# Performance work log

Hardware: AMD Instinct MI355X
Metric: run time of the kernel (lower is better)

## Reference

```python
import jax, jax.numpy as jnp
import numpy as np

B, S, D, H = 4, 2048, 1024, 16
DK = D // H


def setup_inputs() -> dict:
    key = jax.random.key(0)
    ks = jax.random.split(key, 16)
    s = 0.02
    inp = {
        "Q": jax.random.normal(ks[0], (B, S, D), jnp.float32),
        "K": jax.random.normal(ks[1], (B, S, D), jnp.float32),
        "V": jax.random.normal(ks[2], (B, S, D), jnp.float32),
        "mask": jax.random.randint(ks[3], (B, 1, S, S), 0, 2, jnp.int32),
        "wq": jax.random.normal(ks[4], (D, D), jnp.float32) * s,
        "bq": jnp.zeros((D,), jnp.float32),
        "wk": jax.random.normal(ks[5], (D, D), jnp.float32) * s,
        "bk": jnp.zeros((D,), jnp.float32),
        "wv": jax.random.normal(ks[6], (D, D), jnp.float32) * s,
        "bv": jnp.zeros((D,), jnp.float32),
        "wo": jax.random.normal(ks[7], (D, D), jnp.float32) * s,
        "bo": jnp.zeros((D,), jnp.float32),
        "na_q_w": jax.random.normal(ks[8], (DK, DK), jnp.float32) * 0.1,
        "na_q_b": jnp.zeros((DK,), jnp.float32),
        "na_k_w": jax.random.normal(ks[9], (DK, DK), jnp.float32) * 0.1,
        "na_k_b": jnp.zeros((DK,), jnp.float32),
        "temperature": jnp.ones((H, 1, 1), jnp.float32),
        "rms_w": jnp.ones((D,), jnp.float32),
    }
    return inp


def _split_heads(x):
    # [B,S,D] -> [B,H,S,DK]
    return x.reshape(B, S, H, DK).transpose(0, 2, 1, 3)


def reference(Q, K, V, mask, wq, bq, wk, bk, wv, bv, wo, bo,
              na_q_w, na_q_b, na_k_w, na_k_b, temperature, rms_w):
    q = _split_heads(Q @ wq.T + bq)
    k = _split_heads(K @ wk.T + bk)
    v = _split_heads(V @ wv.T + bv)
    # NeuralAttention: tanh-transformed Q,K then scaled dot product
    qn = jnp.tanh(q @ na_q_w.T + na_q_b)
    kn = jnp.tanh(k @ na_k_w.T + na_k_b)
    scores = jnp.einsum("bhqd,bhkd->bhqk", qn, kn) / (DK ** 0.5)
    scores = scores / temperature  # [H,1,1] broadcasts over [B,H,S,S]
    scores = jnp.where(mask == 0, jnp.float32(-1e9), scores)
    attn = jax.nn.softmax(scores, axis=-1)
    ctx = jnp.einsum("bhqk,bhkd->bhqd", attn, v)
    out = ctx.transpose(0, 2, 1, 3).reshape(B, S, D) @ wo.T + bo
    # RMSNorm
    out = out * jax.lax.rsqrt(jnp.mean(out * out, axis=-1, keepdims=True) + 1e-8) * rms_w
    return out
```

## Files before the change

kernel.cpp:

```cpp
#include <hip/hip_runtime.h>
#include <hip/hip_bf16.h>

constexpr int Bc  = 4;
constexpr int Sc  = 2048;
constexpr int Dc  = 1024;
constexpr int Hc  = 16;
constexpr int DKc = 64;
constexpr int Mc  = Bc * Sc;

typedef __bf16 bf16x8 __attribute__((ext_vector_type(8)));
typedef float  f32x4  __attribute__((ext_vector_type(4)));
typedef unsigned short ushort_t;

#define DEV __device__ __forceinline__

DEV unsigned short f2bf(float f) {
    unsigned u = __builtin_bit_cast(unsigned, f);
    u += 0x7FFFu + ((u >> 16) & 1u);
    return (unsigned short)(u >> 16);
}
DEV unsigned pack2(float a, float b) {
    return (unsigned)f2bf(a) | ((unsigned)f2bf(b) << 16);
}
DEV void gl16(const void* g, void* l) {
    __builtin_amdgcn_global_load_lds((const __attribute__((address_space(1))) unsigned int*)g,
                                     (__attribute__((address_space(3))) unsigned int*)l, 16, 0, 0);
}
DEV f32x4 mfma16(bf16x8 a, bf16x8 b, f32x4 c) {
    return __builtin_amdgcn_mfma_f32_16x16x32_bf16(a, b, c, 0, 0, 0);
}
DEV unsigned spread4(unsigned x) {
    x = (x | (x << 12)) & 0x000F000Fu;
    x = (x | (x << 6))  & 0x03030303u;
    x = (x | (x << 3))  & 0x11111111u;
    return x;
}


__global__ __launch_bounds__(256) void fold_w2(const float* __restrict__ naqw,
                                               const float* __restrict__ wq,
                                               unsigned short* __restrict__ wqf,
                                               const float* __restrict__ nakw,
                                               const float* __restrict__ wk,
                                               unsigned short* __restrict__ wkf,
                                               const float* __restrict__ bq,
                                               const float* __restrict__ naqb,
                                               float* __restrict__ bqf,
                                               const float* __restrict__ bk,
                                               const float* __restrict__ nakb,
                                               float* __restrict__ bkf) {
    const int colg = blockIdx.x, h = blockIdx.y, z = blockIdx.z;
    if (z == 2) {
        if (h >= 2) return;
        const float* na = h ? nakw : naqw;
        const float* b  = h ? bk : bq;
        const float* nb = h ? nakb : naqb;
        float* out      = h ? bkf : bqf;
        int idx = colg * 256 + threadIdx.x;
        if (idx >= Dc) return;
        int hh = idx >> 6, i = idx & 63;
        float acc = nb[i];
        for (int t = 0; t < DKc; ++t) acc += na[i * DKc + t] * b[hh * DKc + t];
        out[idx] = acc;
        return;
    }
    const float* na = z ? nakw : naqw;
    const float* w  = z ? wk : wq;
    unsigned short* out = z ? wkf : wqf;
    const int col = colg * 256 + threadIdx.x;

    __shared__ float nal[64 * 64];
    for (int i = threadIdx.x; i < 4096; i += 256) nal[i] = na[i];

    float wr[64];
#pragma unroll
    for (int t = 0; t < 64; ++t) wr[t] = w[(h * 64 + t) * Dc + col];
    __syncthreads();

    for (int i = 0; i < 64; ++i) {
        float acc = 0.f;
#pragma unroll
        for (int t = 0; t < 64; ++t) acc += nal[i * 64 + t] * wr[t];
        out[(h * 64 + i) * Dc + col] = f2bf(acc);
    }
}

constexpr int CONVB = (3 * Mc * Dc + 2 * Dc * Dc) / 8 / 256;
constexpr int MASKB = Bc * Sc * Sc / 1024;
__global__ __launch_bounds__(256) void conv_mask(const float* __restrict__ Q,
                                                 const float* __restrict__ K,
                                                 const float* __restrict__ V,
                                                 const float* __restrict__ wv,
                                                 const float* __restrict__ wo,
                                                 ushort_t* __restrict__ qb,
                                                 ushort_t* __restrict__ kb,
                                                 ushort_t* __restrict__ vb,
                                                 ushort_t* __restrict__ wvf,
                                                 ushort_t* __restrict__ wof,
                                                 const int* __restrict__ m,
                                                 unsigned* __restrict__ mbits) {
    const int bid = blockIdx.x;
    const int tid = threadIdx.x;
    if (bid < CONVB) {
        size_t i = ((size_t)bid * 256 + tid) * 8;
        constexpr size_t N = (size_t)Mc * Dc;
        constexpr size_t W = (size_t)Dc * Dc;
        const float* src; ushort_t* dst; size_t off;
        if      (i < N)         { src = Q;  dst = qb;  off = i; }
        else if (i < 2 * N)     { src = K;  dst = kb;  off = i - N; }
        else if (i < 3 * N)     { src = V;  dst = vb;  off = i - 2 * N; }
        else if (i < 3 * N + W) { src = wv; dst = wvf; off = i - 3 * N; }
        else                    { src = wo; dst = wof; off = i - 3 * N - W; }
        float4 a = *(const float4*)(src + off), b = *(const float4*)(src + off + 4);
        uint4 o;
        o.x = pack2(a.x, a.y); o.y = pack2(a.z, a.w);
        o.z = pack2(b.x, b.y); o.w = pack2(b.z, b.w);
        *(uint4*)(dst + off) = o;
    } else {
        const int mb = bid - CONVB;
        const size_t p0 = ((size_t)mb * 256 + tid) * 4;
        const int ing = (int)(p0 & 63);
        const int nat = (((ing >> 4) & 1) << 5) | (((ing >> 2) & 3) << 3)
                      | (((ing >> 5) & 1) << 2);
        const int4 mv = *(const int4*)(m + ((p0 & ~(size_t)63) | (size_t)nat));
        unsigned nib = (unsigned)(mv.x != 0) | ((unsigned)(mv.y != 0) << 1)
                     | ((unsigned)(mv.z != 0) << 2) | ((unsigned)(mv.w != 0) << 3);
        unsigned long long bal0 = __ballot((nib & 1u) != 0);
        unsigned long long bal1 = __ballot((nib & 2u) != 0);
        unsigned long long bal2 = __ballot((nib & 4u) != 0);
        unsigned long long bal3 = __ballot((nib & 8u) != 0);
        const int lane = tid & 63, s = tid >> 6;
        const int sh8 = (lane & 7) * 8;
        unsigned bb0 = (unsigned)(bal0 >> sh8) & 0xFFu;
        unsigned bb1 = (unsigned)(bal1 >> sh8) & 0xFFu;
        unsigned bb2 = (unsigned)(bal2 >> sh8) & 0xFFu;
        unsigned bb3 = (unsigned)(bal3 >> sh8) & 0xFFu;
        unsigned word = spread4(bb0) | (spread4(bb1) << 1)
                      | (spread4(bb2) << 2) | (spread4(bb3) << 3);
        if (lane < 8) mbits[(size_t)mb * 32 + s * 8 + lane] = word;
    }
}

template <int EPI, int SWZ>
__global__ __launch_bounds__(256) void gemm_bt(const ushort_t* __restrict__ A,
                                               const ushort_t* __restrict__ B,
                                               const float* __restrict__ bias,
                                               void* __restrict__ outp,
                                               int Mdim, int Ndim, int Kdim,
                                               const float* __restrict__ temp,
                                               const ushort_t* __restrict__ A2,
                                               const ushort_t* __restrict__ B2,
                                               const float* __restrict__ bias2,
                                               void* __restrict__ outp2) {
    __shared__ __align__(16) unsigned char As[2][16384];
    __shared__ __align__(16) unsigned char Bs[2][16384];

    int zz = 0;
    if constexpr (EPI == 4) {
        zz = blockIdx.z;
        if (zz) { A = A2; B = B2; bias = bias2; outp = outp2; }
    }

    int bx = blockIdx.x, by = blockIdx.y;
    if constexpr (SWZ != 0) {
        int nwg = gridDim.x * gridDim.y;
        int L = by * gridDim.x + bx;
        int cpx = nwg >> 3;
        int orig = (L & 7) * cpx + (L >> 3);
        if constexpr (SWZ == 1) { bx = orig % gridDim.x; by = orig / gridDim.x; }
        else                    { by = orig % gridDim.y; bx = orig / gridDim.y; }
    }

    const int tid = threadIdx.x, lane = tid & 63, wave = tid >> 6;
    const int wr = wave >> 1, wc = wave & 1;
    const int q = lane & 15, g = lane >> 4;
    const int m0 = by * 128, n0 = bx * 128;

    const int strow = lane >> 3, stcol = (lane & 7) * 8;
    const ushort_t* Ab = A + (size_t)(m0 + strow) * Kdim + stcol;
    const ushort_t* Bb = B + (size_t)(n0 + strow) * Kdim + stcol;

    f32x4 acc[4][4] = {};
    const int nK = Kdim >> 6;

#pragma unroll
    for (int i = 0; i < 4; ++i) {
        const int ro = (wave * 4 + i) * 8;
        gl16(Ab + (size_t)ro * Kdim, As[0] + (wave * 4 + i) * 1024);
        gl16(Bb + (size_t)ro * Kdim, Bs[0] + (wave * 4 + i) * 1024);
    }
    __syncthreads();

    for (int kt = 0; kt < nK; ++kt) {
        const int cur = kt & 1;
        if (kt + 1 < nK) {
            const int k1 = (kt + 1) << 6;
#pragma unroll
            for (int i = 0; i < 4; ++i) {
                const int ro = (wave * 4 + i) * 8;
                gl16(Ab + (size_t)ro * Kdim + k1, As[cur ^ 1] + (wave * 4 + i) * 1024);
                gl16(Bb + (size_t)ro * Kdim + k1, Bs[cur ^ 1] + (wave * 4 + i) * 1024);
            }
        }
#pragma unroll
        for (int s = 0; s < 2; ++s) {
            const int cb = s * 64 + g * 16;
            bf16x8 a[4], b[4];
#pragma unroll
            for (int m = 0; m < 4; ++m)
                a[m] = *(const bf16x8*)(As[cur] + (wr * 64 + m * 16 + q) * 128 + cb);
#pragma unroll
            for (int n = 0; n < 4; ++n)
                b[n] = *(const bf16x8*)(Bs[cur] + (wc * 64 + n * 16 + q) * 128 + cb);
#pragma unroll
            for (int m = 0; m < 4; ++m)
#pragma unroll
                for (int n = 0; n < 4; ++n)
                    acc[m][n] = mfma16(a[m], b[n], acc[m][n]);
        }
        __syncthreads();
    }

#pragma unroll
    for (int m = 0; m < 4; ++m)
#pragma unroll
        for (int n = 0; n < 4; ++n) {
            int gn = n0 + wc * 64 + n * 16 + q;
            float sc_h = 1.f;
            if constexpr (EPI == 0 || EPI == 4) {
                if (EPI == 0 || zz == 0)
                    sc_h = 0.18033688011112042f * __builtin_amdgcn_rcpf(temp[gn >> 6]);
            }
#pragma unroll
            for (int r = 0; r < 4; ++r) {
                int gm = m0 + wr * 64 + m * 16 + (g << 2) + r;
                float v = acc[m][n][r];
                if constexpr (EPI == 0 || EPI == 3 || EPI == 4) {
                    v = tanhf(v + bias[gn]);
                    int b = gm >> 11, s = gm & 2047, hh = gn >> 6, dk = gn & 63;
                    bool qmode = (EPI == 0) || (EPI == 4 && zz == 0);
                    if (qmode) {
                        ((unsigned short*)outp)[(((size_t)(b * Hc + hh)) * Sc + s) * DKc + dk] = f2bf(v * sc_h);
                    } else {
                        int kt2 = s >> 7, nr = s & 127;
                        int prow = (nr & 64) | (((nr >> 5) & 1) << 4) | (((nr >> 3) & 3) << 2)
                                 | (((nr >> 2) & 1) << 5) | (nr & 3);
                        int eofs = ((dk * 2) ^ ((prow & 7) << 4)) >> 1;
                        size_t idx = ((size_t)(b * Hc + hh)) * Sc * DKc + (size_t)kt2 * 8192 + prow * 64 + eofs;
                        ((unsigned short*)outp)[idx] = f2bf(v);
                    }
                } else if constexpr (EPI == 1) {
                    v += bias[gm];
                    int hh = gm >> 6, dk = gm & 63, b = gn >> 11, s = gn & 2047;
                    int kt2 = s >> 7, kloc = s & 127;
                    int eofs = ((kloc * 2) ^ ((dk & 7) << 4)) >> 1;
                    size_t idx = ((size_t)(b * Hc + hh)) * Sc * DKc + (size_t)kt2 * 8192 + dk * 128 + eofs;
                    ((unsigned short*)outp)[idx] = f2bf(v);
                } else {
                    v += bias[gn];
                    ((float*)outp)[(size_t)gm * Ndim + gn] = v;
                }
            }
        }
}

__global__ __launch_bounds__(512, 2) void attn_k(const ushort_t* __restrict__ qn,
                                                 const ushort_t* __restrict__ kn,
                                                 const ushort_t* __restrict__ vtp,
                                                 const unsigned* __restrict__ mbits,
                                                 ushort_t* __restrict__ ctxb) {
    __shared__ __align__(16) unsigned char Kl[2][16384];
    __shared__ __align__(16) unsigned char Vl[2][16384];

    const int tid = threadIdx.x, lane = tid & 63, wave = tid >> 6;
    const int q = lane & 15, g = lane >> 4;

    const int wg = blockIdx.x;
    const int orig = (wg & 7) * 64 + (wg >> 3);
    const int qt = orig & 7, h = (orig >> 3) & 15, b = orig >> 7;
    const int q0 = qt * 256;
    const int qr0 = q0 + wave * 32 + q;
    const size_t headoff = ((size_t)(b * Hc + h)) * Sc * DKc;

    const unsigned char* Ksrc = (const unsigned char*)(kn + headoff);
    const unsigned char* Vsrc = (const unsigned char*)(vtp + headoff);
    const int so = wave * 1024 + lane * 16;
    const int ld = wave * 1024;

    bf16x8 qf[2][2];
    {
        const ushort_t* p0 = qn + headoff + (size_t)qr0 * DKc + g * 8;
        qf[0][0] = *(const bf16x8*)p0;
        qf[0][1] = *(const bf16x8*)(p0 + 32);
        qf[1][0] = *(const bf16x8*)(p0 + 16 * DKc);
        qf[1][1] = *(const bf16x8*)(p0 + 16 * DKc + 32);
    }
    const unsigned* mr0 = mbits + ((size_t)b * Sc + qr0) * (Sc / 32);
    const unsigned* mr1 = mr0 + 16 * (Sc / 32);

    bf16x8 ones;
#pragma unroll
    for (int i = 0; i < 8; ++i) ones[i] = (__bf16)1.0f;

    f32x4 ctxa[2][4] = {};
    f32x4 lacc[2] = {};
    const int swz = (q & 7) << 4;
    const int sh = g << 2;

    gl16(Ksrc + so,        &Kl[0][ld]);
    gl16(Ksrc + 8192 + so, &Kl[0][8192 + ld]);
    gl16(Vsrc + so,        &Vl[0][ld]);
    gl16(Vsrc + 8192 + so, &Vl[0][8192 + ld]);
    __syncthreads();

    for (int kt = 0; kt < Sc / 128; ++kt) {
        const int cur = kt & 1;
        if (kt < Sc / 128 - 1) {
            const unsigned char* ks = Ksrc + (kt + 1) * 16384;
            const unsigned char* vs = Vsrc + (kt + 1) * 16384;
            gl16(ks + so,        &Kl[cur ^ 1][ld]);
            gl16(ks + 8192 + so, &Kl[cur ^ 1][8192 + ld]);
            gl16(vs + so,        &Vl[cur ^ 1][ld]);
            gl16(vs + 8192 + so, &Vl[cur ^ 1][8192 + ld]);
        }
        unsigned mwq[2][4];
        {
            uint4 t0 = *(const uint4*)(mr0 + kt * 4);
            uint4 t1 = *(const uint4*)(mr1 + kt * 4);
            mwq[0][0] = t0.x >> sh; mwq[0][1] = t0.y >> sh;
            mwq[0][2] = t0.z >> sh; mwq[0][3] = t0.w >> sh;
            mwq[1][0] = t1.x >> sh; mwq[1][1] = t1.y >> sh;
            mwq[1][2] = t1.z >> sh; mwq[1][3] = t1.w >> sh;
        }
        const unsigned char* Kb = Kl[cur];
        const unsigned char* Vb = Vl[cur];

#pragma unroll
        for (int kh = 0; kh < 2; ++kh) {
            f32x4 s0[4] = {}, s1[4] = {};
            __builtin_amdgcn_s_setprio(1);
#pragma unroll
            for (int f = 0; f < 4; ++f) {
                const int ro = (kh * 64 + f * 16 + q) * 128;
                bf16x8 a0 = *(const bf16x8*)(Kb + ro + ((g * 16) ^ swz));
                bf16x8 a1 = *(const bf16x8*)(Kb + ro + ((64 + g * 16) ^ swz));
                s0[f] = mfma16(a0, qf[0][0], s0[f]);
                s0[f] = mfma16(a1, qf[0][1], s0[f]);
                s1[f] = mfma16(a0, qf[1][0], s1[f]);
                s1[f] = mfma16(a1, qf[1][1], s1[f]);
            }
            __builtin_amdgcn_s_setprio(0);

#pragma unroll
            for (int f = 0; f < 4; ++f) {
                unsigned w0 = mwq[0][kh * 2 + (f >> 1)];
                unsigned w1 = mwq[1][kh * 2 + (f >> 1)];
#pragma unroll
                for (int r = 0; r < 4; ++r) {
                    const unsigned bitc = 1u << (((f & 1) << 4) + r);
                    float v0 = (w0 & bitc) ? s0[f][r] : -1e30f;
                    float v1 = (w1 & bitc) ? s1[f][r] : -1e30f;
                    s0[f][r] = __builtin_amdgcn_exp2f(v0);
                    s1[f][r] = __builtin_amdgcn_exp2f(v1);
                }
            }

            bf16x8 pa0[2], pa1[2];
#pragma unroll
            for (int cs = 0; cs < 2; ++cs)
#pragma unroll
                for (int r = 0; r < 4; ++r) {
                    pa0[cs][r]     = (__bf16)s0[cs][r];
                    pa0[cs][4 + r] = (__bf16)s0[cs + 2][r];
                    pa1[cs][r]     = (__bf16)s1[cs][r];
                    pa1[cs][4 + r] = (__bf16)s1[cs + 2][r];
                }

            __builtin_amdgcn_s_setprio(1);
#pragma unroll
            for (int cs = 0; cs < 2; ++cs) {
                const int csg = kh * 2 + cs;
                lacc[0] = mfma16(pa0[cs], ones, lacc[0]);
                lacc[1] = mfma16(pa1[cs], ones, lacc[1]);
#pragma unroll
                for (int j = 0; j < 4; ++j) {
                    bf16x8 vb = *(const bf16x8*)(Vb + (j * 16 + q) * 256 + ((csg * 64 + g * 16) ^ swz));
                    ctxa[0][j] = mfma16(pa0[cs], vb, ctxa[0][j]);
                    ctxa[1][j] = mfma16(pa1[cs], vb, ctxa[1][j]);
                }
            }
            __builtin_amdgcn_s_setprio(0);
        }
        __syncthreads();
    }

#pragma unroll
    for (int qg = 0; qg < 2; ++qg) {
        f32x4 linv;
#pragma unroll
        for (int r = 0; r < 4; ++r) linv[r] = __builtin_amdgcn_rcpf(lacc[qg][r]);
#pragma unroll
        for (int j = 0; j < 4; ++j)
#pragma unroll
            for (int r = 0; r < 4; ++r) {
                int srow = q0 + wave * 32 + qg * 16 + (g << 2) + r;
                int col = h * DKc + j * 16 + q;
                float v = ctxa[qg][j][r] * linv[r];
                ctxb[((size_t)b * Sc + srow) * Dc + col] = __builtin_bit_cast(unsigned short, (__bf16)v);
            }
    }
}

__global__ __launch_bounds__(256) void rmsnorm_k(float* __restrict__ out,
                                                 const float* __restrict__ w) {
    const int row = blockIdx.x, tid = threadIdx.x;
    float4* p = (float4*)(out + (size_t)row * Dc) + tid;
    float4 v = *p;
    float ss = v.x * v.x + v.y * v.y + v.z * v.z + v.w * v.w;
#pragma unroll
    for (int o = 32; o >= 1; o >>= 1) ss += __shfl_xor(ss, o);
    __shared__ float sm[4];
    if ((tid & 63) == 0) sm[tid >> 6] = ss;
    __syncthreads();
    float tot = sm[0] + sm[1] + sm[2] + sm[3];
    float r = rsqrtf(tot * (1.f / Dc) + 1e-8f);
    float4 wv = *((const float4*)w + tid);
    v.x *= r * wv.x; v.y *= r * wv.y; v.z *= r * wv.z; v.w *= r * wv.w;
    *p = v;
}

extern "C" void kernel_launch(void* const* d_in, const int* in_sizes, int n_in,
                              void* d_out, int out_size, void* d_ws, size_t ws_size,
                              hipStream_t stream) {
    (void)in_sizes; (void)n_in; (void)out_size; (void)ws_size;
    const float* Q    = (const float*)d_in[0];
    const float* K    = (const float*)d_in[1];
    const float* V    = (const float*)d_in[2];
    const int*   mask = (const int*)  d_in[3];
    const float* wq   = (const float*)d_in[4];
    const float* bq   = (const float*)d_in[5];
    const float* wk   = (const float*)d_in[6];
    const float* bk   = (const float*)d_in[7];
    const float* wv   = (const float*)d_in[8];
    const float* bv   = (const float*)d_in[9];
    const float* wo   = (const float*)d_in[10];
    const float* bo   = (const float*)d_in[11];
    const float* naqw = (const float*)d_in[12];
    const float* naqb = (const float*)d_in[13];
    const float* nakw = (const float*)d_in[14];
    const float* nakb = (const float*)d_in[15];
    const float* temp = (const float*)d_in[16];
    const float* rmsw = (const float*)d_in[17];

    char* ws = (char*)d_ws;
    size_t off = 0;
    auto take = [&](size_t n) { char* p = ws + off; off += (n + 255) & ~(size_t)255; return p; };
    unsigned short* vtb  = (unsigned short*)take((size_t)Mc * Dc * 2);
    unsigned short* qb   = (unsigned short*)take((size_t)Mc * Dc * 2);
    unsigned short* kb   = (unsigned short*)take((size_t)Mc * Dc * 2);
    unsigned short* vb   = (unsigned short*)take((size_t)Mc * Dc * 2);
    unsigned short* qnb  = (unsigned short*)take((size_t)Mc * Dc * 2);
    unsigned short* knb  = (unsigned short*)take((size_t)Mc * Dc * 2);
    unsigned short* wqf  = (unsigned short*)take((size_t)Dc * Dc * 2);
    unsigned short* wkf  = (unsigned short*)take((size_t)Dc * Dc * 2);
    unsigned short* wvf  = (unsigned short*)take((size_t)Dc * Dc * 2);
    unsigned short* wof  = (unsigned short*)take((size_t)Dc * Dc * 2);
    float*    bqf   = (float*)take(Dc * 4);
    float*    bkf   = (float*)take(Dc * 4);
    unsigned* mbits = (unsigned*)take((size_t)Bc * Sc * (Sc / 32) * 4);
    unsigned short* ctxb = kb;

    fold_w2<<<dim3(4, 16, 3), 256, 0, stream>>>(naqw, wq, wqf, nakw, wk, wkf,
                                                bq, naqb, bqf, bk, nakb, bkf);
    conv_mask<<<dim3(CONVB + MASKB), 256, 0, stream>>>(Q, K, V, wv, wo,
                                                       qb, kb, vb, wvf, wof,
                                                       mask, mbits);

    gemm_bt<1, 2><<<dim3(Mc / 128, Dc / 128), 256, 0, stream>>>(
        wvf, vb, bv, vtb, Dc, Mc, Dc, nullptr,
        nullptr, nullptr, nullptr, nullptr);
    gemm_bt<4, 1><<<dim3(Dc / 128, Mc / 128, 2), 256, 0, stream>>>(
        qb, wqf, bqf, qnb, Mc, Dc, Dc, temp,
        kb, wkf, bkf, knb);

    attn_k<<<dim3(512), 512, 0, stream>>>(qnb, knb, vtb, mbits, ctxb);

    gemm_bt<2, 1><<<dim3(Dc / 128, Mc / 128), 256, 0, stream>>>(
        ctxb, wof, bo, d_out, Mc, Dc, Dc, nullptr,
        nullptr, nullptr, nullptr, nullptr);
    rmsnorm_k<<<dim3(Mc), 256, 0, stream>>>((float*)d_out, rmsw);
}
```

Measured before the change: 288.2 us.

## Use 256x256 tiles with 512 threads for fused Q/K projection GEMM

```diff
diff --git a/kernel.cpp b/kernel.cpp
--- a/kernel.cpp
+++ b/kernel.cpp
@@ -146,23 +146,12 @@
                                                const ushort_t* __restrict__ B,
                                                const float* __restrict__ bias,
                                                void* __restrict__ outp,
-                                               int Mdim, int Ndim, int Kdim,
-                                               const float* __restrict__ temp,
-                                               const ushort_t* __restrict__ A2,
-                                               const ushort_t* __restrict__ B2,
-                                               const float* __restrict__ bias2,
-                                               void* __restrict__ outp2) {
+                                               int Mdim, int Ndim, int Kdim) {
     __shared__ __align__(16) unsigned char As[2][16384];
     __shared__ __align__(16) unsigned char Bs[2][16384];
 
-    int zz = 0;
-    if constexpr (EPI == 4) {
-        zz = blockIdx.z;
-        if (zz) { A = A2; B = B2; bias = bias2; outp = outp2; }
-    }
-
     int bx = blockIdx.x, by = blockIdx.y;
-    if constexpr (SWZ != 0) {
+    {
         int nwg = gridDim.x * gridDim.y;
         int L = by * gridDim.x + bx;
         int cpx = nwg >> 3;
@@ -226,30 +215,11 @@
 #pragma unroll
         for (int n = 0; n < 4; ++n) {
             int gn = n0 + wc * 64 + n * 16 + q;
-            float sc_h = 1.f;
-            if constexpr (EPI == 0 || EPI == 4) {
-                if (EPI == 0 || zz == 0)
-                    sc_h = 0.18033688011112042f * __builtin_amdgcn_rcpf(temp[gn >> 6]);
-            }
 #pragma unroll
             for (int r = 0; r < 4; ++r) {
                 int gm = m0 + wr * 64 + m * 16 + (g << 2) + r;
                 float v = acc[m][n][r];
-                if constexpr (EPI == 0 || EPI == 3 || EPI == 4) {
-                    v = tanhf(v + bias[gn]);
-                    int b = gm >> 11, s = gm & 2047, hh = gn >> 6, dk = gn & 63;
-                    bool qmode = (EPI == 0) || (EPI == 4 && zz == 0);
-                    if (qmode) {
-                        ((unsigned short*)outp)[(((size_t)(b * Hc + hh)) * Sc + s) * DKc + dk] = f2bf(v * sc_h);
-                    } else {
-                        int kt2 = s >> 7, nr = s & 127;
-                        int prow = (nr & 64) | (((nr >> 5) & 1) << 4) | (((nr >> 3) & 3) << 2)
-                                 | (((nr >> 2) & 1) << 5) | (nr & 3);
-                        int eofs = ((dk * 2) ^ ((prow & 7) << 4)) >> 1;
-                        size_t idx = ((size_t)(b * Hc + hh)) * Sc * DKc + (size_t)kt2 * 8192 + prow * 64 + eofs;
-                        ((unsigned short*)outp)[idx] = f2bf(v);
-                    }
-                } else if constexpr (EPI == 1) {
+                if constexpr (EPI == 1) {
                     v += bias[gm];
                     int hh = gm >> 6, dk = gm & 63, b = gn >> 11, s = gn & 2047;
                     int kt2 = s >> 7, kloc = s & 127;
@@ -259,6 +229,101 @@
                 } else {
                     v += bias[gn];
                     ((float*)outp)[(size_t)gm * Ndim + gn] = v;
+                }
+            }
+        }
+}
+
+__global__ __launch_bounds__(512, 2) void gemm_qk256(const ushort_t* __restrict__ qb,
+                                                     const ushort_t* __restrict__ wqf,
+                                                     const float* __restrict__ bqf,
+                                                     ushort_t* __restrict__ qnb,
+                                                     const ushort_t* __restrict__ kb,
+                                                     const ushort_t* __restrict__ wkf,
+                                                     const float* __restrict__ bkf,
+                                                     ushort_t* __restrict__ knb,
+                                                     const float* __restrict__ temp) {
+    __shared__ __align__(16) unsigned char As[2][32768];
+    __shared__ __align__(16) unsigned char Bs[2][32768];
+
+    const int zz = blockIdx.z;
+    const ushort_t* A = zz ? kb : qb;
+    const ushort_t* B = zz ? wkf : wqf;
+    const float* bias = zz ? bkf : bqf;
+
+    int L = blockIdx.y * gridDim.x + blockIdx.x;
+    int orig = (L & 7) * 16 + (L >> 3);
+    int bx = orig & 3, by = orig >> 2;
+
+    const int tid = threadIdx.x, lane = tid & 63, wave = tid >> 6;
+    const int wr = wave >> 2, wc = wave & 3;
+    const int q = lane & 15, g = lane >> 4;
+    const int m0 = by * 256, n0 = bx * 256;
+
+    const int strow = lane >> 3, stcol = (lane & 7) * 8;
+    const ushort_t* Ab = A + (size_t)(m0 + strow) * Dc + stcol;
+    const ushort_t* Bb = B + (size_t)(n0 + strow) * Dc + stcol;
+
+    f32x4 acc[8][4] = {};
+    constexpr int nK = Dc >> 6;
+
+#define STAGE256(buf, k0)                                                       \
+    {                                                                           \
+        _Pragma("unroll")                                                       \
+        for (int i = 0; i < 4; ++i) {                                           \
+            const int j = wave * 4 + i;                                         \
+            gl16(Ab + (size_t)(j * 8) * Dc + (k0), As[buf] + j * 1024);         \
+            gl16(Bb + (size_t)(j * 8) * Dc + (k0), Bs[buf] + j * 1024);         \
+        }                                                                       \
+    }
+
+    STAGE256(0, 0);
+    __syncthreads();
+
+    for (int kt = 0; kt < nK; ++kt) {
+        const int cur = kt & 1;
+        if (kt + 1 < nK) STAGE256(cur ^ 1, (kt + 1) << 6);
+#pragma unroll
+        for (int s = 0; s < 2; ++s) {
+            const int cb = s * 64 + g * 16;
+            bf16x8 a[8], b[4];
+#pragma unroll
+            for (int m = 0; m < 8; ++m)
+                a[m] = *(const bf16x8*)(As[cur] + (wr * 128 + m * 16 + q) * 128 + cb);
+#pragma unroll
+            for (int n = 0; n < 4; ++n)
+                b[n] = *(const bf16x8*)(Bs[cur] + (wc * 64 + n * 16 + q) * 128 + cb);
+#pragma unroll
+            for (int m = 0; m < 8; ++m)
+#pragma unroll
+                for (int n = 0; n < 4; ++n)
+                    acc[m][n] = mfma16(a[m], b[n], acc[m][n]);
+        }
+        __syncthreads();
+    }
+#undef STAGE256
+
+#pragma unroll
+    for (int m = 0; m < 8; ++m)
+#pragma unroll
+        for (int n = 0; n < 4; ++n) {
+            int gn = n0 + wc * 64 + n * 16 + q;
+            float sc_h = 1.f;
+            if (zz == 0) sc_h = 0.18033688011112042f * __builtin_amdgcn_rcpf(temp[gn >> 6]);
+#pragma unroll
+            for (int r = 0; r < 4; ++r) {
+                int gm = m0 + wr * 128 + m * 16 + (g << 2) + r;
+                float v = tanhf(acc[m][n][r] + bias[gn]);
+                int b = gm >> 11, s = gm & 2047, hh = gn >> 6, dk = gn & 63;
+                if (zz == 0) {
+                    qnb[(((size_t)(b * Hc + hh)) * Sc + s) * DKc + dk] = f2bf(v * sc_h);
+                } else {
+                    int kt2 = s >> 7, nr = s & 127;
+                    int prow = (nr & 64) | (((nr >> 5) & 1) << 4) | (((nr >> 3) & 3) << 2)
+                             | (((nr >> 2) & 1) << 5) | (nr & 3);
+                    int eofs = ((dk * 2) ^ ((prow & 7) << 4)) >> 1;
+                    size_t idx = ((size_t)(b * Hc + hh)) * Sc * DKc + (size_t)kt2 * 8192 + prow * 64 + eofs;
+                    knb[idx] = f2bf(v);
                 }
             }
         }
@@ -477,16 +542,13 @@
                                                        mask, mbits);
 
     gemm_bt<1, 2><<<dim3(Mc / 128, Dc / 128), 256, 0, stream>>>(
-        wvf, vb, bv, vtb, Dc, Mc, Dc, nullptr,
-        nullptr, nullptr, nullptr, nullptr);
-    gemm_bt<4, 1><<<dim3(Dc / 128, Mc / 128, 2), 256, 0, stream>>>(
-        qb, wqf, bqf, qnb, Mc, Dc, Dc, temp,
-        kb, wkf, bkf, knb);
+        wvf, vb, bv, vtb, Dc, Mc, Dc);
+    gemm_qk256<<<dim3(4, 32, 2), 512, 0, stream>>>(
+        qb, wqf, bqf, qnb, kb, wkf, bkf, knb, temp);
 
     attn_k<<<dim3(512), 512, 0, stream>>>(qnb, knb, vtb, mbits, ctxb);
 
     gemm_bt<2, 1><<<dim3(Dc / 128, Mc / 128), 256, 0, stream>>>(
-        ctxb, wof, bo, d_out, Mc, Dc, Dc, nullptr,
-        nullptr, nullptr, nullptr, nullptr);
+        ctxb, wof, bo, d_out, Mc, Dc, Dc);
     rmsnorm_k<<<dim3(Mc), 256, 0, stream>>>((float*)d_out, rmsw);
 }
```

Measured after the change: 289.1 us. Within noise of the previous version (+0.3%).
